# Performance work log

Measured on AMD Instinct MI355X. Metric: run time of the kernel, lower is better.

Reference implementation:

```python
import jax, jax.numpy as jnp
import numpy as np

B, T, E, H = 8, 2048, 1024, 128


def setup_inputs() -> dict:
    key = jax.random.key(0)
    kx, kk, kq, kv = jax.random.split(key, 4)
    x = jax.random.normal(kx, (B, T, E), dtype=jnp.float32)
    # nn.Linear(E, H, bias=False) weights, stored as (E, H) so y = x @ W
    scale = 0.02
    Wk = jax.random.normal(kk, (E, H), dtype=jnp.float32) * scale
    Wq = jax.random.normal(kq, (E, H), dtype=jnp.float32) * scale
    Wv = jax.random.normal(kv, (E, H), dtype=jnp.float32) * scale
    return {"x": x, "Wk": Wk, "Wq": Wq, "Wv": Wv}


def reference(x, Wk, Wq, Wv):
    # x: (B,T,E) -> k,q,v: (B,T,H)
    k = x @ Wk
    q = x @ Wq
    v = x @ Wv
    # att[b,t,s] = q[b,t] . k[b,s]
    att = jnp.einsum('bth,bsh->bts', q, k)
    # original: att / head_norm, head_norm = 1/sqrt(H)  => multiply by sqrt(H)
    att = att * jnp.sqrt(jnp.float32(H))
    tril = jnp.tril(jnp.ones((T, T), dtype=bool))
    att = jnp.where(tril, att, -jnp.inf)
    # original softmax over dim=1 (query axis), NOT the key axis
    att = jax.nn.softmax(att, axis=1)
    return att @ v  # (B,T,H)
```

## Files before the change

kernel.cpp:

```cpp
#include <hip/hip_runtime.h>
#include <math.h>

#define Bn 8
#define Tn 2048
#define En 1024
#define Hn 128
#define SQRTH_LOG2E (11.313708498984761f * 1.4426950408889634f)

typedef __attribute__((ext_vector_type(8))) short short8;
typedef __attribute__((ext_vector_type(8))) _Float16 half8;
typedef __attribute__((ext_vector_type(4))) short short4v;
typedef __attribute__((ext_vector_type(4))) float float4v;

#define MFMA16(a, b, c)  __builtin_amdgcn_mfma_f32_16x16x32_bf16((a), (b), (c), 0, 0, 0)
#define MFMA16F(a, b, c) __builtin_amdgcn_mfma_f32_16x16x32_f16((a), (b), (c), 0, 0, 0)
#define EXP2(x) __builtin_amdgcn_exp2f(x)

static __device__ __forceinline__ unsigned short f2bf(float f) {
    unsigned u = __float_as_uint(f);
    u += 0x7FFFu + ((u >> 16) & 1u);
    return (unsigned short)(u >> 16);
}
static __device__ __forceinline__ unsigned short f2h(float f) {
    _Float16 h = (_Float16)f;
    union { _Float16 v; unsigned short u; } c; c.v = h; return c.u;
}

static __device__ __forceinline__ void gll16(const unsigned short* g, unsigned short* l) {
    __builtin_amdgcn_global_load_lds(
        (const __attribute__((address_space(1))) unsigned int*)g,
        (__attribute__((address_space(3))) unsigned int*)l, 16, 0, 0);
}


__global__ __launch_bounds__(256) void prep_kernel(
    const float* __restrict__ x,
    const float* __restrict__ Wq, const float* __restrict__ Wk, const float* __restrict__ Wv,
    unsigned short* __restrict__ xt, unsigned short* __restrict__ wtt)
{
    if (blockIdx.x < 8192) {
        int g = blockIdx.x * 256 + threadIdx.x;
        int kc8 = g & 3;
        int rr = (g >> 2) & 63;
        int ks = (g >> 8) & 31;
        int mt = g >> 13;
        size_t src = ((size_t)mt * 64 + rr) * En + ks * 32 + kc8 * 8;
        float4v f0 = *(const float4v*)(x + src);
        float4v f1 = *(const float4v*)(x + src + 4);
        short8 h;
#pragma unroll
        for (int j = 0; j < 4; j++) {
            h[j] = (short)f2h(f0[j]);
            h[j + 4] = (short)f2h(f1[j]);
        }
        size_t d = (size_t)(g >> 2) * 32 + (size_t)(kc8 ^ (rr & 3)) * 8;
        *(short8*)(xt + d) = h;
    } else {
        int t = (blockIdx.x - 8192) * 256 + threadIdx.x;
        int kc8 = t & 3;
        int hh = (t >> 2) & 127;
        int ks = (t >> 9) & 31;
        int z = t >> 14;
        const float* W = (z == 0) ? Wq : ((z == 1) ? Wk : Wv);
        short8 h8;
#pragma unroll
        for (int j = 0; j < 8; j++) {
            int e = ks * 32 + kc8 * 8 + j;
            h8[j] = (short)f2h(W[(size_t)e * Hn + hh]);
        }
        size_t d = (((size_t)z * 32 + ks) * 4096) + (size_t)hh * 32
                 + (size_t)(kc8 ^ (hh & 3)) * 8;
        *(short8*)(wtt + d) = h8;
    }
}

__global__ __launch_bounds__(256) void proj_kernel(
    const unsigned short* __restrict__ xt, const unsigned short* __restrict__ wtt,
    unsigned short* __restrict__ qf, unsigned short* __restrict__ kf,
    unsigned short* __restrict__ vtt)
{
    __shared__ __align__(16) unsigned short lds[2][6144];
    int z = blockIdx.y;
    int mt = blockIdx.x;
    int tid = threadIdx.x;
    int wave = tid >> 6, lane = tid & 63;
    int c15 = lane & 15, kg = lane >> 4;
    int sb = c15 & 3;
    int mrow = wave >> 1, ncol = wave & 1;

    const unsigned short* A0 = xt + (size_t)mt * 32 * 2048;
    const unsigned short* B0 = wtt + (size_t)z * 32 * 4096;

    float4v acc[2][4];
#pragma unroll
    for (int i = 0; i < 2; i++)
#pragma unroll
        for (int j = 0; j < 4; j++) acc[i][j] = (float4v)0.0f;

    const unsigned short* gcur[3];
    int lbo[3];
    int gstep[3];
#pragma unroll
    for (int i = 0; i < 3; i++) {
        int ch = wave * 3 + i;
        if (ch < 4) { gcur[i] = A0 + ch * 512;       lbo[i] = ch * 512;        gstep[i] = 2048; }
        else        { gcur[i] = B0 + (ch - 4) * 512; lbo[i] = 2048 + (ch - 4) * 512; gstep[i] = 4096; }
    }
    int lo8 = lane * 8;

    auto stage = [&](int buf) {
        unsigned short* Lb = lds[0] + buf * 6144;
#pragma unroll
        for (int i = 0; i < 3; i++) {
            gll16(gcur[i] + lo8, Lb + lbo[i] + lo8);
            gcur[i] += gstep[i];
        }
    };

    stage(0);

    for (int ks = 0; ks < 32; ks++) {
        __syncthreads();
        if (ks + 1 < 32) stage((ks + 1) & 1);
        const unsigned short* Lb = lds[ks & 1];

        half8 ah[2], bh[4];
#pragma unroll
        for (int mi = 0; mi < 2; mi++) {
            int row = mrow * 32 + mi * 16 + c15;
            ah[mi] = *(const half8*)(Lb + row * 32 + (kg ^ sb) * 8);
        }
#pragma unroll
        for (int ni = 0; ni < 4; ni++) {
            int row = ncol * 64 + ni * 16 + c15;
            bh[ni] = *(const half8*)(Lb + 2048 + row * 32 + (kg ^ sb) * 8);
        }
#pragma unroll
        for (int mi = 0; mi < 2; mi++)
#pragma unroll
            for (int ni = 0; ni < 4; ni++)
                acc[mi][ni] = MFMA16F(ah[mi], bh[ni], acc[mi][ni]);
    }

    if (z < 2) {
        unsigned short* oh = (z == 0) ? qf : kf;
#pragma unroll
        for (int mi = 0; mi < 2; mi++) {
#pragma unroll
            for (int ni = 0; ni < 4; ni++) {
                int h = ncol * 64 + ni * 16 + c15;
#pragma unroll
                for (int r = 0; r < 4; r++) {
                    int t = mt * 64 + mrow * 32 + mi * 16 + kg * 4 + r;
                    size_t o = (size_t)t * Hn + (((h >> 3) ^ (t & 15)) << 3) + (h & 7);
                    oh[o] = f2h(acc[mi][ni][r]);
                }
            }
        }
    } else {
        int b = mt >> 5;
#pragma unroll
        for (int mi = 0; mi < 2; mi++) {
            int t0 = (mt & 31) * 64 + mrow * 32 + mi * 16 + kg * 4;
            int sc = t0 >> 5, so = t0 & 31;
#pragma unroll
            for (int ni = 0; ni < 4; ni++) {
                int h = ncol * 64 + ni * 16 + c15;
                short4v pk;
#pragma unroll
                for (int r = 0; r < 4; r++) pk[r] = (short)f2bf(acc[mi][ni][r]);
                int so2 = ((((so >> 3) ^ ((h >> 1) & 3))) << 3) | (so & 7);
                *(short4v*)(vtt + (((size_t)b * 64 + sc) * 128 + h) * 32 + so2) = pk;
            }
        }
    }
}

__global__ __launch_bounds__(256) void stats_part_kernel(
    const unsigned short* __restrict__ qf, const unsigned short* __restrict__ kf,
    float* __restrict__ m_part, float* __restrict__ l_part)
{
    __shared__ __align__(16) unsigned short lds[4096];
    int tid = threadIdx.x;
    int wave = tid >> 6, lane = tid & 63;
    int c15 = lane & 15, kg = lane >> 4;
    int b = blockIdx.x;

    int rem = (int)blockIdx.y, sj, nch = 1;
    for (sj = 0; sj < 32; sj++) {
        nch = ((31 - sj) >> 2) + 1;
        if (rem < nch) break;
        rem -= nch;
    }
    int ci = rem;
    int c0 = 2 * sj;
    int len = 64 - c0;
    int cbase = len / nch, ext = len % nch;
    int cs = c0 + ci * cbase + (ci < ext ? ci : ext);
    int ce = cs + cbase + (ci < ext ? 1 : 0);

    int s_base = sj * 64 + wave * 16;

    half8 a[4];
    {
        int s = s_base + c15;
        const unsigned short* kr = kf + ((size_t)(b * Tn + s)) * Hn;
#pragma unroll
        for (int st = 0; st < 4; st++) {
            int off = ((st * 4 + kg) ^ c15) * 8;
            a[st] = *(const half8*)(kr + off);
        }
    }
    float m[4], l[4];
#pragma unroll
    for (int r = 0; r < 4; r++) { m[r] = -3.0e38f; l[r] = 0.0f; }

    auto stage = [&](int c) {
        const unsigned short* Qf = qf + ((size_t)b * Tn + c * 32) * Hn;
        int lo8 = lane * 8;
#pragma unroll
        for (int i = 0; i < 2; i++) {
            int ch = wave * 2 + i;
            gll16(Qf + ch * 512 + lo8, lds + ch * 512 + lo8);
        }
    };

    for (int c = cs; c < ce; c++) {
        stage(c);
        __syncthreads();
        float4v av[2];
#pragma unroll
        for (int half = 0; half < 2; half++) {
            int tl = half * 16 + c15;
            float4v a1 = (float4v)0.0f;
#pragma unroll
            for (int st = 0; st < 4; st++) {
                int off = tl * 128 + ((st * 4 + kg) ^ c15) * 8;
                half8 bh = *(const half8*)(lds + off);
                a1 = MFMA16F(a[st], bh, a1);
            }
            av[half] = a1;
        }
        int t0 = c * 32 + c15;
        int t1 = c * 32 + 16 + c15;
#pragma unroll
        for (int r = 0; r < 4; r++) {
            int s_row = s_base + kg * 4 + r;
            float v0 = av[0][r] * SQRTH_LOG2E;
            float v1 = av[1][r] * SQRTH_LOG2E;
            bool val0 = (t0 >= s_row), val1 = (t1 >= s_row);
            float c0v = val0 ? v0 : -3.0e38f;
            float c1v = val1 ? v1 : -3.0e38f;
            float mn = fmaxf(m[r], fmaxf(c0v, c1v));
            l[r] = l[r] * EXP2(m[r] - mn)
                 + (val0 ? EXP2(v0 - mn) : 0.0f)
                 + (val1 ? EXP2(v1 - mn) : 0.0f);
            m[r] = mn;
        }
        __syncthreads();
    }
#pragma unroll
    for (int mask = 1; mask < 16; mask <<= 1) {
#pragma unroll
        for (int r = 0; r < 4; r++) {
            float mo = __shfl_xor(m[r], mask);
            float lo2 = __shfl_xor(l[r], mask);
            float mn = fmaxf(m[r], mo);
            l[r] = l[r] * EXP2(m[r] - mn) + lo2 * EXP2(mo - mn);
            m[r] = mn;
        }
    }
    if (c15 == 0) {
#pragma unroll
        for (int r = 0; r < 4; r++) {
            int sl = wave * 16 + kg * 4 + r;
            size_t d = ((((size_t)b * 32 + sj) * 8 + ci) * 64) + sl;
            m_part[d] = m[r];
            l_part[d] = l[r];
        }
    }
}

__global__ __launch_bounds__(256) void out_part_kernel(
    const unsigned short* __restrict__ qf, const unsigned short* __restrict__ kf,
    const unsigned short* __restrict__ vtt,
    const float* __restrict__ m_part, const float* __restrict__ l_part,
    float* __restrict__ part_out)
{
    __shared__ __align__(16) unsigned short lds[8192];
    __shared__ __align__(16) unsigned short pbuf[4][16][40];
    __shared__ float2 mlbuf[256];
    int tid = threadIdx.x;
    int wave = tid >> 6, lane = tid & 63;
    int c15 = lane & 15, kg = lane >> 4;
    int b = blockIdx.x;

    int rem = (int)blockIdx.y, tj, nch = 1;
    for (tj = 31; tj >= 0; tj--) {
        nch = (tj >> 2) + 1;
        if (rem < nch) break;
        rem -= nch;
    }
    int ci = rem;
    int len = 2 * tj + 2;
    int cbase = len / nch, ext = len % nch;
    int cs = ci * cbase + (ci < ext ? ci : ext);
    int ce = cs + cbase + (ci < ext ? 1 : 0);

    {
        int ncols = (ce - cs) * 32;
        if (tid < ncols) {
            int s = cs * 32 + tid;
            int sj2 = s >> 6, sl2 = s & 63;
            int nchs = ((31 - sj2) >> 2) + 1;
            size_t base = (((size_t)b * 32 + sj2) * 8) * 64 + sl2;
            float M = m_part[base];
            float L = l_part[base];
            for (int cj = 1; cj < nchs; cj++) {
                float mi = m_part[base + (size_t)cj * 64];
                float li = l_part[base + (size_t)cj * 64];
                float mn = fmaxf(M, mi);
                L = L * EXP2(M - mn) + li * EXP2(mi - mn);
                M = mn;
            }
            float2 ml; ml.x = M; ml.y = 1.0f / L;
            mlbuf[tid] = ml;
        }
    }

    int t_base = tj * 64 + wave * 16;

    half8 qa[4];
    {
        int t = t_base + c15;
        const unsigned short* qr = qf + ((size_t)(b * Tn + t)) * Hn;
#pragma unroll
        for (int st = 0; st < 4; st++) {
            int off = ((st * 4 + kg) ^ c15) * 8;
            qa[st] = *(const half8*)(qr + off);
        }
    }
    float4v oacc[8];
#pragma unroll
    for (int i = 0; i < 8; i++) oacc[i] = (float4v)0.0f;

    auto stage = [&](int c) {
        const unsigned short* Kf = kf + ((size_t)b * Tn + c * 32) * Hn;
        const unsigned short* Vv = vtt + ((size_t)b * 64 + c) * (128 * 32);
        int lo8 = lane * 8;
#pragma unroll
        for (int i = 0; i < 4; i++) {
            int ch = wave * 4 + i;
            const unsigned short* g;
            unsigned short* ld;
            if (ch < 8) { g = Kf + ch * 512;       ld = lds + ch * 512; }
            else        { g = Vv + (ch - 8) * 512; ld = lds + 4096 + (ch - 8) * 512; }
            gll16(g + lo8, ld + lo8);
        }
    };

    for (int c = cs; c < ce; c++) {
        stage(c);
        __syncthreads();
#pragma unroll
        for (int half = 0; half < 2; half++) {
            int s16 = c * 32 + half * 16;
            int sl = half * 16 + c15;
            float4v a1 = (float4v)0.0f;
#pragma unroll
            for (int st = 0; st < 4; st++) {
                int off = sl * 128 + ((st * 4 + kg) ^ c15) * 8;
                half8 bh = *(const half8*)(lds + off);
                a1 = MFMA16F(qa[st], bh, a1);
            }
            float2 mlv = mlbuf[(c - cs) * 32 + sl];
#pragma unroll
            for (int r = 0; r < 4; r++) {
                int t = t_base + kg * 4 + r;
                float attv = a1[r] * SQRTH_LOG2E;
                float earg = fminf(attv - mlv.x, 0.0f);
                float p = (t >= s16 + c15) ? EXP2(earg) * mlv.y : 0.0f;
                pbuf[wave][kg * 4 + r][c15 + half * 16] = f2bf(p);
            }
        }
        short8 pa = *(const short8*)&pbuf[wave][c15][kg * 8];
#pragma unroll
        for (int nt = 0; nt < 8; nt++) {
            int voff = (nt * 16 + c15) * 32 + ((kg ^ ((c15 >> 1) & 3)) * 8);
            short8 vb = *(const short8*)(lds + 4096 + voff);
            oacc[nt] = MFMA16(pa, vb, oacc[nt]);
        }
        __syncthreads();
    }
    float* po = part_out + ((((size_t)b * 32 + tj) * 8 + ci) * 64) * 128;
#pragma unroll
    for (int nt = 0; nt < 8; nt++) {
        int h = nt * 16 + c15;
#pragma unroll
        for (int r = 0; r < 4; r++) {
            int tl = wave * 16 + kg * 4 + r;
            po[(size_t)tl * 128 + h] = oacc[nt][r];
        }
    }
}

__global__ __launch_bounds__(256) void out_combine_kernel(
    const float* __restrict__ part_out, float* __restrict__ out)
{
    int g = blockIdx.x * 256 + threadIdx.x;
    int h4 = g & 31;
    int t = (g >> 5) & 2047;
    int b = g >> 16;
    int tj = t >> 6, tl = t & 63;
    int nch = (tj >> 2) + 1;
    const float4v* p = (const float4v*)(part_out
        + ((((size_t)b * 32 + tj) * 8) * 64 + tl) * 128) + h4;
    float4v acc = p[0];
    for (int ci = 1; ci < nch; ci++) acc += p[(size_t)ci * 2048];
    *((float4v*)(out + ((size_t)b * Tn + t) * Hn) + h4) = acc;
}

extern "C" void kernel_launch(void* const* d_in, const int* in_sizes, int n_in,
                              void* d_out, int out_size, void* d_ws, size_t ws_size,
                              hipStream_t stream)
{
    (void)in_sizes; (void)n_in; (void)out_size; (void)ws_size;
    const float* x  = (const float*)d_in[0];
    const float* Wk = (const float*)d_in[1];
    const float* Wq = (const float*)d_in[2];
    const float* Wv = (const float*)d_in[3];
    float* out = (float*)d_out;

    const size_t NQ = (size_t)Bn * Tn * Hn;
    const size_t NX = (size_t)Bn * Tn * En;
    unsigned short* qf  = (unsigned short*)d_ws;
    unsigned short* qlo = qf + NQ;
    unsigned short* kf  = qlo + NQ;
    unsigned short* klo = kf + NQ;
    unsigned short* vtt  = klo + NQ;
    unsigned short* xt   = vtt + NQ;
    unsigned short* xt_lo = xt + NX;
    unsigned short* wtt  = xt_lo + NX;
    unsigned short* wtt_lo = wtt + (size_t)3 * Hn * En;

    float* part_out = (float*)xt;
    float* m_part   = (float*)wtt;
    float* l_part   = (float*)wtt_lo;

    prep_kernel<<<dim3(8384), 256, 0, stream>>>(x, Wq, Wk, Wv, xt, wtt);
    proj_kernel<<<dim3(256, 3), 256, 0, stream>>>(xt, wtt, qf, kf, vtt);
    stats_part_kernel<<<dim3(Bn, 144), 256, 0, stream>>>(qf, kf, m_part, l_part);
    out_part_kernel<<<dim3(Bn, 144), 256, 0, stream>>>(qf, kf, vtt,
                                                       m_part, l_part, part_out);
    out_combine_kernel<<<dim3(2048), 256, 0, stream>>>(part_out, out);
}
```

Measured before the change: 169.3 us.

## Fuse partial-output combine into out_part via last-block atomic counter

Removes the separate out_combine kernel. Each out_part block now takes a per-tile atomic ticket after a threadfence, and the last chunk block for a tile sums all partial outputs and writes the final result. The prep kernel gains one extra block that zeroes the counters. This saves a launch and its tail, at the cost of a serialized reduction done by one block per tile and extra fences.

```diff
diff --git a/kernel.cpp b/kernel.cpp
--- a/kernel.cpp
+++ b/kernel.cpp
@@ -36,7 +36,8 @@
 __global__ __launch_bounds__(256) void prep_kernel(
     const float* __restrict__ x,
     const float* __restrict__ Wq, const float* __restrict__ Wk, const float* __restrict__ Wv,
-    unsigned short* __restrict__ xt, unsigned short* __restrict__ wtt)
+    unsigned short* __restrict__ xt, unsigned short* __restrict__ wtt,
+    unsigned int* __restrict__ tile_cnt)
 {
     if (blockIdx.x < 8192) {
         int g = blockIdx.x * 256 + threadIdx.x;
@@ -55,7 +56,7 @@
         }
         size_t d = (size_t)(g >> 2) * 32 + (size_t)(kc8 ^ (rr & 3)) * 8;
         *(short8*)(xt + d) = h;
-    } else {
+    } else if (blockIdx.x < 8384) {
         int t = (blockIdx.x - 8192) * 256 + threadIdx.x;
         int kc8 = t & 3;
         int hh = (t >> 2) & 127;
@@ -71,6 +72,8 @@
         size_t d = (((size_t)z * 32 + ks) * 4096) + (size_t)hh * 32
                  + (size_t)(kc8 ^ (hh & 3)) * 8;
         *(short8*)(wtt + d) = h8;
+    } else {
+        tile_cnt[threadIdx.x] = 0u;
     }
 }
 
@@ -285,11 +288,13 @@
     const unsigned short* __restrict__ qf, const unsigned short* __restrict__ kf,
     const unsigned short* __restrict__ vtt,
     const float* __restrict__ m_part, const float* __restrict__ l_part,
-    float* __restrict__ part_out)
+    float* __restrict__ part_out, unsigned int* __restrict__ tile_cnt,
+    float* __restrict__ out)
 {
     __shared__ __align__(16) unsigned short lds[8192];
     __shared__ __align__(16) unsigned short pbuf[4][16][40];
     __shared__ float2 mlbuf[256];
+    __shared__ unsigned int oldc;
     int tid = threadIdx.x;
     int wave = tid >> 6, lane = tid & 63;
     int c15 = lane & 15, kg = lane >> 4;
@@ -402,22 +407,22 @@
             po[(size_t)tl * 128 + h] = oacc[nt][r];
         }
     }
-}
-
-__global__ __launch_bounds__(256) void out_combine_kernel(
-    const float* __restrict__ part_out, float* __restrict__ out)
-{
-    int g = blockIdx.x * 256 + threadIdx.x;
-    int h4 = g & 31;
-    int t = (g >> 5) & 2047;
-    int b = g >> 16;
-    int tj = t >> 6, tl = t & 63;
-    int nch = (tj >> 2) + 1;
-    const float4v* p = (const float4v*)(part_out
-        + ((((size_t)b * 32 + tj) * 8) * 64 + tl) * 128) + h4;
-    float4v acc = p[0];
-    for (int ci = 1; ci < nch; ci++) acc += p[(size_t)ci * 2048];
-    *((float4v*)(out + ((size_t)b * Tn + t) * Hn) + h4) = acc;
+
+    __threadfence();
+    __syncthreads();
+    if (tid == 0) oldc = atomicAdd(&tile_cnt[b * 32 + tj], 1u);
+    __syncthreads();
+    if (oldc == (unsigned)(nch - 1)) {
+        __threadfence();
+        const float4v* pp = (const float4v*)(part_out
+            + ((((size_t)b * 32 + tj) * 8) * 64) * 128);
+        float* ob = out + ((size_t)b * Tn + tj * 64) * Hn;
+        for (int i = tid; i < 2048; i += 256) {
+            float4v acc2 = pp[i];
+            for (int cj = 1; cj < nch; cj++) acc2 += pp[(size_t)cj * 2048 + i];
+            *((float4v*)ob + i) = acc2;
+        }
+    }
 }
 
 extern "C" void kernel_launch(void* const* d_in, const int* in_sizes, int n_in,
@@ -446,11 +451,12 @@
     float* part_out = (float*)xt;
     float* m_part   = (float*)wtt;
     float* l_part   = (float*)wtt_lo;
-
-    prep_kernel<<<dim3(8384), 256, 0, stream>>>(x, Wq, Wk, Wv, xt, wtt);
+    unsigned int* tile_cnt = (unsigned int*)(l_part + (size_t)Bn * 32 * 8 * 64);
+
+    prep_kernel<<<dim3(8385), 256, 0, stream>>>(x, Wq, Wk, Wv, xt, wtt, tile_cnt);
     proj_kernel<<<dim3(256, 3), 256, 0, stream>>>(xt, wtt, qf, kf, vtt);
     stats_part_kernel<<<dim3(Bn, 144), 256, 0, stream>>>(qf, kf, m_part, l_part);
     out_part_kernel<<<dim3(Bn, 144), 256, 0, stream>>>(qf, kf, vtt,
-                                                       m_part, l_part, part_out);
-    out_combine_kernel<<<dim3(2048), 256, 0, stream>>>(part_out, out);
-}
+                                                       m_part, l_part,
+                                                       part_out, tile_cnt, out);
+}
```

Measured after the change: 386.9 us. +128.5%, slower.
